# Performance work log

Measured on AMD Instinct MI355X. Metric: run time of the kernel, lower is better.

Reference implementation:

```python
import jax, jax.numpy as jnp
import numpy as np

B, D, H = 16384, 1024, 8
DH = D // H
LN_EPS = 1e-5


def setup_inputs() -> dict:
    key = jax.random.key(0)
    ks = jax.random.split(key, 16)
    s = 0.02  # weight init scale to keep softmax logits sane
    d = {}
    d['f40'] = jax.random.normal(ks[0], (B, D), jnp.float32)
    d['f100'] = jax.random.normal(ks[1], (B, D), jnp.float32)
    d['f200'] = jax.random.normal(ks[2], (B, D), jnp.float32)
    d['f400'] = jax.random.normal(ks[3], (B, D), jnp.float32)
    d['mag_emb'] = jax.random.normal(ks[4], (4, D), jnp.float32)
    i = 5
    for mag in ('100', '200', '400'):
        d[f'in_w_{mag}'] = jax.random.normal(ks[i], (3 * D, D), jnp.float32) * s
        d[f'in_b_{mag}'] = jnp.zeros((3 * D,), jnp.float32)
        d[f'out_w_{mag}'] = jax.random.normal(ks[i + 1], (D, D), jnp.float32) * s
        d[f'out_b_{mag}'] = jnp.zeros((D,), jnp.float32)
        d[f'ln_w_{mag}'] = jnp.ones((D,), jnp.float32)
        d[f'ln_b_{mag}'] = jnp.zeros((D,), jnp.float32)
        i += 2
    return d


def _layer_norm(x, w, b):
    m = jnp.mean(x, axis=-1, keepdims=True)
    v = jnp.mean(jnp.square(x - m), axis=-1, keepdims=True)
    return (x - m) * jax.lax.rsqrt(v + LN_EPS) * w + b


def _mha(q, kv, in_w, in_b, out_w, out_b):
    # q: [B,1,D], kv: [B,S,D]. Matches torch nn.MultiheadAttention (batch_first).
    S = kv.shape[1]
    wq, wk, wv = jnp.split(in_w, 3, axis=0)
    bq, bk, bv = jnp.split(in_b, 3)
    qp = (q @ wq.T + bq).reshape(B, 1, H, DH)
    kp = (kv @ wk.T + bk).reshape(B, S, H, DH)
    vp = (kv @ wv.T + bv).reshape(B, S, H, DH)
    scores = jnp.einsum('bqhd,bkhd->bhqk', qp, kp) / np.sqrt(DH).astype(np.float32)
    attn = jax.nn.softmax(scores, axis=-1)           # [B,H,1,S]
    out = jnp.einsum('bhqk,bkhd->bqhd', attn, vp).reshape(B, 1, D)
    out = (out @ out_w.T + out_b)[:, 0, :]           # [B,D]
    return out, attn.mean(axis=1)                     # weights averaged over heads: [B,1,S]


def reference(f40, f100, f200, f400, mag_emb,
              in_w_100, in_b_100, out_w_100, out_b_100, ln_w_100, ln_b_100,
              in_w_200, in_b_200, out_w_200, out_b_200, ln_w_200, ln_b_200,
              in_w_400, in_b_400, out_w_400, out_b_400, ln_w_400, ln_b_400):
    feats = (f40, f100, f200, f400)
    enh = [f + mag_emb[i] for i, f in enumerate(feats)]
    level_params = [
        (in_w_100, in_b_100, out_w_100, out_b_100, ln_w_100, ln_b_100),
        (in_w_200, in_b_200, out_w_200, out_b_200, ln_w_200, ln_b_200),
        (in_w_400, in_b_400, out_w_400, out_b_400, ln_w_400, ln_b_400),
    ]
    hier = [enh[0]]
    attn_maps = []
    for i, (iw, ib, ow, ob, lw, lb) in enumerate(level_params):
        ctx = jnp.stack(hier, axis=1)                 # [B, i+1, D]
        attended, w = _mha(enh[i + 1][:, None, :], ctx, iw, ib, ow, ob)
        fused = _layer_norm(enh[i + 1] + attended, lw, lb)
        hier.append(fused)
        attn_maps.append(w)
    return (hier[0], hier[1], hier[2], hier[3], attn_maps[0], attn_maps[1], attn_maps[2])
```

## Files before the change

### kernel.cpp

```cpp
#include <hip/hip_runtime.h>

typedef unsigned short u16;
typedef unsigned int u32;

#define NB 16384
#define ND 1024
static constexpr size_t BD = (size_t)NB * ND;
static constexpr size_t DD = (size_t)ND * ND;

typedef __attribute__((ext_vector_type(8))) short s16x8;
typedef __attribute__((ext_vector_type(4))) float f32x4;

__device__ __forceinline__ u16 f2bf(float f) {
  union { float f; u32 u; } v; v.f = f;
  return (u16)((v.u + 0x7fffu + ((v.u >> 16) & 1u)) >> 16);
}
__device__ __forceinline__ float asf(u32 u) {
  union { u32 u; float f; } v; v.u = u; return v.f;
}
__device__ __forceinline__ uint2 pack4(float a, float b, float c, float d) {
  uint2 p;
  p.x = (u32)f2bf(a) | ((u32)f2bf(b) << 16);
  p.y = (u32)f2bf(c) | ((u32)f2bf(d) << 16);
  return p;
}
__device__ __forceinline__ void load16bf(const u16* p, float* o) {
  const uint4* q = (const uint4*)p;
  uint4 u0 = q[0], u1 = q[1];
  u32 w[8] = {u0.x, u0.y, u0.z, u0.w, u1.x, u1.y, u1.z, u1.w};
#pragma unroll
  for (int i = 0; i < 8; ++i) {
    o[2 * i]     = asf(w[i] << 16);
    o[2 * i + 1] = asf(w[i] & 0xffff0000u);
  }
}
__device__ __forceinline__ void store16bf(u16* p, const float* o) {
  uint4 u0, u1;
  u0.x = (u32)f2bf(o[0])  | ((u32)f2bf(o[1])  << 16);
  u0.y = (u32)f2bf(o[2])  | ((u32)f2bf(o[3])  << 16);
  u0.z = (u32)f2bf(o[4])  | ((u32)f2bf(o[5])  << 16);
  u0.w = (u32)f2bf(o[6])  | ((u32)f2bf(o[7])  << 16);
  u1.x = (u32)f2bf(o[8])  | ((u32)f2bf(o[9])  << 16);
  u1.y = (u32)f2bf(o[10]) | ((u32)f2bf(o[11]) << 16);
  u1.z = (u32)f2bf(o[12]) | ((u32)f2bf(o[13]) << 16);
  u1.w = (u32)f2bf(o[14]) | ((u32)f2bf(o[15]) << 16);
  ((uint4*)p)[0] = u0;
  ((uint4*)p)[1] = u1;
}

#define G2L(gp, lp) __builtin_amdgcn_global_load_lds( \
    (__attribute__((address_space(1))) void*)(void*)(gp), \
    (__attribute__((address_space(3))) void*)(lp), 16, 0, 0)

template<int BF16_OUT>
__device__ __forceinline__ void gemm_core(
    const u16* __restrict__ A, const u16* __restrict__ Bm,
    const float* __restrict__ bias, void* __restrict__ Cp,
    int N, int K, int ldc, int row0, int col0)
{
  __shared__ __align__(16) u16 lA[128 * 64];
  __shared__ __align__(16) u16 lB[128 * 64];
  const int tid  = threadIdx.x;
  const int wave = tid >> 6;
  const int lane = tid & 63;
  const int wm = (wave >> 1) * 64;
  const int wn = (wave & 1) * 64;
  const int fr = lane & 15;
  const int fq = lane >> 4;
  const int srow = tid >> 3;
  const int scol = ((tid & 7) ^ (srow & 7)) * 8;

  f32x4 acc[4][4];
#pragma unroll
  for (int i = 0; i < 4; ++i)
#pragma unroll
    for (int j = 0; j < 4; ++j) acc[i][j] = (f32x4){0.f, 0.f, 0.f, 0.f};

  const u16* Abase = A  + (size_t)(row0 + srow) * K + scol;
  const u16* Bbase = Bm + (size_t)(col0 + srow) * K + scol;
  u16* lAw = lA + wave * 512;
  u16* lBw = lB + wave * 512;
  const int rsw = (fr & 7) << 3;

  for (int kt = 0; kt < K; kt += 64) {
#pragma unroll
    for (int c = 0; c < 4; ++c) {
      G2L(Abase + (size_t)(c * 32) * K + kt, lAw + c * 2048);
      G2L(Bbase + (size_t)(c * 32) * K + kt, lBw + c * 2048);
    }
    __syncthreads();

#pragma unroll
    for (int kk = 0; kk < 2; ++kk) {
      s16x8 af[4], bfr[4];
#pragma unroll
      for (int i = 0; i < 4; ++i) {
        af[i]  = *(const s16x8*)&lA[(wm + i * 16 + fr) * 64 + ((kk * 32 + fq * 8) ^ rsw)];
        bfr[i] = *(const s16x8*)&lB[(wn + i * 16 + fr) * 64 + ((kk * 32 + fq * 8) ^ rsw)];
      }
#pragma unroll
      for (int i = 0; i < 4; ++i)
#pragma unroll
        for (int j = 0; j < 4; ++j)
          acc[i][j] = __builtin_amdgcn_mfma_f32_16x16x32_bf16(af[i], bfr[j], acc[i][j], 0, 0, 0);
    }
    __syncthreads();
  }

#pragma unroll
  for (int i = 0; i < 4; ++i) {
#pragma unroll
    for (int j = 0; j < 4; ++j) {
      const int col = col0 + wn + j * 16 + fr;
      const float bb = bias ? bias[col] : 0.f;
#pragma unroll
      for (int r = 0; r < 4; ++r) {
        const int row = row0 + wm + i * 16 + fq * 4 + r;
        const float v = acc[i][j][r] + bb;
        if (BF16_OUT) ((u16*)Cp)[(size_t)row * ldc + col] = f2bf(v);
        else          ((float*)Cp)[(size_t)row * ldc + col] = v;
      }
    }
  }
}

__device__ __forceinline__ void swz_rowcol(int* row0, int* col0) {
  const int nwg = gridDim.x * gridDim.y;
  int wgid = blockIdx.y * gridDim.x + blockIdx.x;
  wgid = (wgid & 7) * (nwg >> 3) + (wgid >> 3);
  *row0 = (wgid / gridDim.x) * 128;
  *col0 = (wgid % gridDim.x) * 128;
}

template<int BF16_OUT>
__global__ __launch_bounds__(256, 3) void gemm_bt(
    const u16* __restrict__ A, const u16* __restrict__ Bm,
    const float* __restrict__ bias, void* __restrict__ Cp,
    int N, int K, int ldc)
{
  int row0, col0;
  swz_rowcol(&row0, &col0);
  gemm_core<BF16_OUT>(A, Bm, bias, Cp, N, K, ldc, row0, col0);
}

struct Ptr3 { const u16* a0; const u16* a1; const u16* a2;
              u16* c0; u16* c1; u16* c2; };

__global__ __launch_bounds__(256, 3) void kv_gemm(
    Ptr3 p, const u16* __restrict__ Bm, int K)
{
  int row0, col0;
  swz_rowcol(&row0, &col0);
  const u16* A; u16* C;
  if (blockIdx.z == 0)      { A = p.a0; C = p.c0; }
  else if (blockIdx.z == 1) { A = p.a1; C = p.c1; }
  else                      { A = p.a2; C = p.c2; }
  gemm_core<1>(A, Bm, nullptr, C, 2048, K, 2048, row0, col0);
}

__global__ __launch_bounds__(256) void prep_k(
    const float* __restrict__ f40, const float* __restrict__ f200,
    const float* __restrict__ f400, const float* __restrict__ mag,
    float* __restrict__ out0, u16* __restrict__ h0b,
    u16* __restrict__ e2b, u16* __restrict__ e3b)
{
  const size_t j = ((size_t)blockIdx.x * 256 + threadIdx.x) * 4;
  const int d = (int)(j & 1023);
  float4 m0 = *(const float4*)(mag + d);
  float4 m2 = *(const float4*)(mag + 2 * ND + d);
  float4 m3 = *(const float4*)(mag + 3 * ND + d);
  float4 a  = *(const float4*)(f40 + j);
  float4 c2 = *(const float4*)(f200 + j);
  float4 c3 = *(const float4*)(f400 + j);
  float4 h0;
  h0.x = a.x + m0.x; h0.y = a.y + m0.y; h0.z = a.z + m0.z; h0.w = a.w + m0.w;
  *(float4*)(out0 + j) = h0;
  *(uint2*)(h0b + j) = pack4(h0.x, h0.y, h0.z, h0.w);
  *(uint2*)(e2b + j) = pack4(c2.x + m2.x, c2.y + m2.y, c2.z + m2.z, c2.w + m2.w);
  *(uint2*)(e3b + j) = pack4(c3.x + m3.x, c3.y + m3.y, c3.z + m3.z, c3.w + m3.w);
}

__global__ __launch_bounds__(256) void ones_k(float* __restrict__ p) {
  p[blockIdx.x * 256 + threadIdx.x] = 1.0f;
}

__global__ __launch_bounds__(256) void convw_k(
    const float* __restrict__ iw, const float* __restrict__ ow,
    u16* __restrict__ wbf)
{
  const size_t j = ((size_t)blockIdx.x * 256 + threadIdx.x) * 4;
  const size_t IW = (size_t)3 * ND * ND;
  const float* src = (j < IW) ? (iw + j) : (ow + (j - IW));
  float4 v = *(const float4*)src;
  *(uint2*)(wbf + j) = pack4(v.x, v.y, v.z, v.w);
}

__global__ __launch_bounds__(256) void transpose_bf_k(
    const float* __restrict__ src, u16* __restrict__ dst)
{
  __shared__ float t[32][33];
  const int bx = blockIdx.x & 31, by = blockIdx.x >> 5;
  const int tx = threadIdx.x & 31, ty = threadIdx.x >> 5;
#pragma unroll
  for (int r = 0; r < 4; ++r)
    t[ty + r * 8][tx] = src[(size_t)(by * 32 + ty + r * 8) * ND + bx * 32 + tx];
  __syncthreads();
#pragma unroll
  for (int r = 0; r < 4; ++r)
    dst[(size_t)(bx * 32 + ty + r * 8) * ND + by * 32 + tx] = f2bf(t[tx][ty + r * 8]);
}

__global__ __launch_bounds__(256) void biasfold_k(
    const float* __restrict__ bv, const float* __restrict__ wo,
    const float* __restrict__ bo, float* __restrict__ c0)
{
  const int i = blockIdx.x;
  float s = 0.f;
  for (int k = threadIdx.x; k < ND; k += 256) s += bv[k] * wo[(size_t)i * ND + k];
#pragma unroll
  for (int m = 1; m <= 32; m <<= 1) s += __shfl_xor(s, m, 64);
  __shared__ float red[4];
  const int wv = threadIdx.x >> 6, ln = threadIdx.x & 63;
  if (ln == 0) red[wv] = s;
  __syncthreads();
  if (threadIdx.x == 0) c0[i] = bo[i] + red[0] + red[1] + red[2] + red[3];
}

template<int S>
__global__ __launch_bounds__(256) void attn_k(
    const u16* __restrict__ qp, const u16* __restrict__ kva,
    const u16* __restrict__ kvb, const u16* __restrict__ kvc,
    u16* __restrict__ att, float* __restrict__ amap)
{
  const int wave = threadIdx.x >> 6, lane = threadIdx.x & 63;
  const int b = blockIdx.x * 4 + wave;
  const int d0 = lane * 16;
  const u16* kv[3] = {kva, kvb, kvc};

  float q[16];
  load16bf(qp + (size_t)b * ND + d0, q);

  float sc[S];
  float mx = -1e30f;
#pragma unroll
  for (int s = 0; s < S; ++s) {
    float k[16];
    load16bf(kv[s] + (size_t)b * 2 * ND + d0, k);
    float dot = 0.f;
#pragma unroll
    for (int i = 0; i < 16; ++i) dot += q[i] * k[i];
    dot += __shfl_xor(dot, 1, 64);
    dot += __shfl_xor(dot, 2, 64);
    dot += __shfl_xor(dot, 4, 64);
    sc[s] = dot * 0.08838834764831845f;
    mx = fmaxf(mx, sc[s]);
  }
  float w_[S];
  float den = 0.f;
#pragma unroll
  for (int s = 0; s < S; ++s) { w_[s] = __expf(sc[s] - mx); den += w_[s]; }
  const float inv = 1.f / den;

  float o[16] = {0.f, 0.f, 0.f, 0.f, 0.f, 0.f, 0.f, 0.f,
                 0.f, 0.f, 0.f, 0.f, 0.f, 0.f, 0.f, 0.f};
#pragma unroll
  for (int s = 0; s < S; ++s) {
    float v[16];
    load16bf(kv[s] + (size_t)b * 2 * ND + ND + d0, v);
    const float ws = w_[s] * inv;
#pragma unroll
    for (int i = 0; i < 16; ++i) o[i] += ws * v[i];
  }
  store16bf(att + (size_t)b * ND + d0, o);

#pragma unroll
  for (int s = 0; s < S; ++s) {
    float t = w_[s] * inv;
    t += __shfl_xor(t, 8, 64);
    t += __shfl_xor(t, 16, 64);
    t += __shfl_xor(t, 32, 64);
    if (lane == 0) amap[(size_t)b * S + s] = t * 0.125f;
  }
}

__global__ __launch_bounds__(256) void ln_k(
    const float* __restrict__ f, const float* __restrict__ emb,
    const u16* __restrict__ ob, const float* __restrict__ lw,
    const float* __restrict__ lb, float* __restrict__ outp,
    u16* __restrict__ hbf)
{
  const int b = blockIdx.x, t = threadIdx.x;
  const int d = t * 4;
  const size_t off = (size_t)b * ND + d;
  float4 xf = *(const float4*)(f + off);
  float4 ef = *(const float4*)(emb + d);
  uint2 ov  = *(const uint2*)(ob + off);
  float o0 = asf(ov.x << 16), o1 = asf(ov.x & 0xffff0000u);
  float o2 = asf(ov.y << 16), o3 = asf(ov.y & 0xffff0000u);
  float x0 = xf.x + ef.x + o0;
  float x1 = xf.y + ef.y + o1;
  float x2 = xf.z + ef.z + o2;
  float x3 = xf.w + ef.w + o3;
  float s  = x0 + x1 + x2 + x3;
  float s2 = x0 * x0 + x1 * x1 + x2 * x2 + x3 * x3;
#pragma unroll
  for (int m = 1; m <= 32; m <<= 1) {
    s  += __shfl_xor(s,  m, 64);
    s2 += __shfl_xor(s2, m, 64);
  }
  __shared__ float red[8];
  const int wv = t >> 6, ln = t & 63;
  if (ln == 0) { red[wv] = s; red[4 + wv] = s2; }
  __syncthreads();
  s  = red[0] + red[1] + red[2] + red[3];
  s2 = red[4] + red[5] + red[6] + red[7];
  const float mean = s * (1.f / 1024.f);
  const float var  = s2 * (1.f / 1024.f) - mean * mean;
  const float r = rsqrtf(var + 1e-5f);
  float4 w4 = *(const float4*)(lw + d);
  float4 b4 = *(const float4*)(lb + d);
  float4 y;
  y.x = (x0 - mean) * r * w4.x + b4.x;
  y.y = (x1 - mean) * r * w4.y + b4.y;
  y.z = (x2 - mean) * r * w4.z + b4.z;
  y.w = (x3 - mean) * r * w4.w + b4.w;
  *(float4*)(outp + off) = y;
  if (hbf) *(uint2*)(hbf + off) = pack4(y.x, y.y, y.z, y.w);
}

extern "C" void kernel_launch(void* const* d_in, const int* in_sizes, int n_in,
                              void* d_out, int out_size, void* d_ws, size_t ws_size,
                              hipStream_t stream)
{
  const float* f40  = (const float*)d_in[0];
  const float* f100 = (const float*)d_in[1];
  const float* f200 = (const float*)d_in[2];
  const float* f400 = (const float*)d_in[3];
  const float* mag  = (const float*)d_in[4];
  const float* in_w[3]  = {(const float*)d_in[5],  (const float*)d_in[11], (const float*)d_in[17]};
  const float* in_b[3]  = {(const float*)d_in[6],  (const float*)d_in[12], (const float*)d_in[18]};
  const float* out_w[3] = {(const float*)d_in[7],  (const float*)d_in[13], (const float*)d_in[19]};
  const float* out_b[3] = {(const float*)d_in[8],  (const float*)d_in[14], (const float*)d_in[20]};
  const float* ln_w[3]  = {(const float*)d_in[9],  (const float*)d_in[15], (const float*)d_in[21]};
  const float* ln_b[3]  = {(const float*)d_in[10], (const float*)d_in[16], (const float*)d_in[22]};

  float* out = (float*)d_out;
  char* ws = (char*)d_ws;
  const size_t BF = BD * 2;
  u16* h0b  = (u16*)(ws);
  u16* h1b  = (u16*)(ws + BF);
  u16* h2b  = (u16*)(ws + 2 * BF);
  u16* qpb  = (u16*)(ws + 3 * BF);
  u16* attb = (u16*)(ws + 4 * BF);
  u16* kv0  = (u16*)(ws + 5 * BF);
  u16* kv1  = (u16*)(ws + 7 * BF);
  u16* kv2  = (u16*)(ws + 9 * BF);
  u16* wbf  = (u16*)(ws + 11 * BF);
  float* cs = (float*)(ws + 11 * BF + 8 * (1ull << 20));
  u16* e2b = kv1;
  u16* e3b = kv2;
  u16* hb[3] = {h0b, h1b, h2b};
  const float* f_lvl[3] = {f100, f200, f400};

  dim3 blk(256);
  prep_k<<<dim3((unsigned)(BD / 1024)), blk, 0, stream>>>(f40, f200, f400, mag, out, h0b, e2b, e3b);
  ones_k<<<dim3(NB / 256), blk, 0, stream>>>(out + 4 * BD);

  for (int l = 0; l < 3; ++l) {
    convw_k<<<dim3(4096), blk, 0, stream>>>(in_w[l], out_w[l], wbf);
    const u16* wq  = wbf;
    const u16* wkv = wbf + DD;
    const u16* wo  = wbf + 3 * DD;
    biasfold_k<<<dim3(1024), blk, 0, stream>>>(in_b[l] + 2 * ND, out_w[l], out_b[l], cs);

    if (l == 0) {
      u16* wvT = attb;
      u16* wvo = attb + DD;
      transpose_bf_k<<<dim3(1024), blk, 0, stream>>>(in_w[0] + 2 * DD, wvT);
      gemm_bt<1><<<dim3(8, 8), blk, 0, stream>>>(wo, wvT, nullptr, wvo, ND, ND, ND);
      gemm_bt<1><<<dim3(8, 128), blk, 0, stream>>>(h0b, wvo, cs, qpb, ND, ND, ND);
    } else {
      const u16* eb = (l == 1) ? e2b : e3b;
      gemm_bt<1><<<dim3(8, 128), blk, 0, stream>>>(eb, wq, in_b[l], qpb, ND, ND, ND);
      Ptr3 p = {hb[0], hb[1], hb[2], kv0, kv1, kv2};
      kv_gemm<<<dim3(16, 128, l + 1), blk, 0, stream>>>(p, wkv, ND);
      if (l == 1)
        attn_k<2><<<dim3(NB / 4), blk, 0, stream>>>(qpb, kv0, kv1, kv2, attb,
                                                    out + 4 * BD + NB);
      else
        attn_k<3><<<dim3(NB / 4), blk, 0, stream>>>(qpb, kv0, kv1, kv2, attb,
                                                    out + 4 * BD + 3 * NB);
      gemm_bt<1><<<dim3(8, 128), blk, 0, stream>>>(attb, wo, cs, qpb, ND, ND, ND);
    }
    ln_k<<<dim3(NB), blk, 0, stream>>>(f_lvl[l], mag + (size_t)(l + 1) * ND, qpb,
                                       ln_w[l], ln_b[l], out + (size_t)(l + 1) * BD,
                                       (l < 2) ? hb[l + 1] : nullptr);
  }
}
```

Before: 865.2 us.

## Switch GEMMs to 256x256 tiles with double-buffered LDS pipeline and 512 threads

Replaces the 128x128 single-buffered GEMM core with a 256x256 tile computed by 8 waves, each holding a 128x64 accumulator block. The LDS is double-buffered, with direct global-to-LDS loads issued two k-steps ahead, explicit vmcnt waits and raw barriers replacing __syncthreads. MFMA issue priority is raised during the compute phase. This aims to raise arithmetic intensity and overlap loads with MFMA. In exchange it uses 128KB of LDS and many more accumulator registers per block, which lowers occupancy, and the small 1024x1024 weight GEMM now runs on only 16 blocks.

New measurement: 960.4 us. 11.0% more time.

```diff
diff --git a/kernel.cpp b/kernel.cpp
--- a/kernel.cpp
+++ b/kernel.cpp
@@ -52,71 +52,97 @@
     (__attribute__((address_space(1))) void*)(void*)(gp), \
     (__attribute__((address_space(3))) void*)(lp), 16, 0, 0)
 
+__device__ __forceinline__ void stage256(
+    const u16* __restrict__ Abase, const u16* __restrict__ Bbase,
+    u16* ldsA, u16* ldsB, int wave, int K, int kt)
+{
+#pragma unroll
+  for (int c = 0; c < 4; ++c) {
+    G2L(Abase + (size_t)(c * 64) * K + kt, ldsA + c * 4096 + wave * 512);
+    G2L(Bbase + (size_t)(c * 64) * K + kt, ldsB + c * 4096 + wave * 512);
+  }
+}
+
 template<int BF16_OUT>
-__device__ __forceinline__ void gemm_core(
+__device__ __forceinline__ void gemm256_core(
     const u16* __restrict__ A, const u16* __restrict__ Bm,
     const float* __restrict__ bias, void* __restrict__ Cp,
     int N, int K, int ldc, int row0, int col0)
 {
-  __shared__ __align__(16) u16 lA[128 * 64];
-  __shared__ __align__(16) u16 lB[128 * 64];
+  __shared__ __align__(16) u16 lA[2][256 * 64];
+  __shared__ __align__(16) u16 lB[2][256 * 64];
   const int tid  = threadIdx.x;
   const int wave = tid >> 6;
   const int lane = tid & 63;
-  const int wm = (wave >> 1) * 64;
-  const int wn = (wave & 1) * 64;
+  const int wm = wave >> 2;
+  const int wn = wave & 3;
   const int fr = lane & 15;
   const int fq = lane >> 4;
-  const int srow = tid >> 3;
-  const int scol = ((tid & 7) ^ (srow & 7)) * 8;
-
-  f32x4 acc[4][4];
-#pragma unroll
-  for (int i = 0; i < 4; ++i)
+  const int swr = (fr & 7) * 8;
+
+  const int g_r  = wave * 8 + (lane >> 3);
+  const int scol = ((lane & 7) ^ (lane >> 3)) * 8;
+  const u16* Abase = A  + (size_t)(row0 + g_r) * K + scol;
+  const u16* Bbase = Bm + (size_t)(col0 + g_r) * K + scol;
+
+  f32x4 acc[8][4];
+#pragma unroll
+  for (int i = 0; i < 8; ++i)
 #pragma unroll
     for (int j = 0; j < 4; ++j) acc[i][j] = (f32x4){0.f, 0.f, 0.f, 0.f};
 
-  const u16* Abase = A  + (size_t)(row0 + srow) * K + scol;
-  const u16* Bbase = Bm + (size_t)(col0 + srow) * K + scol;
-  u16* lAw = lA + wave * 512;
-  u16* lBw = lB + wave * 512;
-  const int rsw = (fr & 7) << 3;
-
-  for (int kt = 0; kt < K; kt += 64) {
-#pragma unroll
-    for (int c = 0; c < 4; ++c) {
-      G2L(Abase + (size_t)(c * 32) * K + kt, lAw + c * 2048);
-      G2L(Bbase + (size_t)(c * 32) * K + kt, lBw + c * 2048);
+  const int NT = K >> 6;
+  stage256(Abase, Bbase, &lA[0][0], &lB[0][0], wave, K, 0);
+  stage256(Abase, Bbase, &lA[1][0], &lB[1][0], wave, K, 64);
+
+  for (int t = 0; t < NT; ++t) {
+    if (t < NT - 1) { asm volatile("s_waitcnt vmcnt(8)" ::: "memory"); }
+    else            { asm volatile("s_waitcnt vmcnt(0)" ::: "memory"); }
+    __builtin_amdgcn_sched_barrier(0);
+    __builtin_amdgcn_s_barrier();
+    __builtin_amdgcn_sched_barrier(0);
+
+    const u16* bA = &lA[t & 1][0];
+    const u16* bB = &lB[t & 1][0];
+
+    s16x8 bf_[4][2];
+#pragma unroll
+    for (int ni = 0; ni < 4; ++ni) {
+      const int rb = wn * 64 + ni * 16 + fr;
+      bf_[ni][0] = *(const s16x8*)&bB[rb * 64 + ((fq * 8) ^ swr)];
+      bf_[ni][1] = *(const s16x8*)&bB[rb * 64 + ((32 + fq * 8) ^ swr)];
     }
-    __syncthreads();
-
-#pragma unroll
-    for (int kk = 0; kk < 2; ++kk) {
-      s16x8 af[4], bfr[4];
-#pragma unroll
-      for (int i = 0; i < 4; ++i) {
-        af[i]  = *(const s16x8*)&lA[(wm + i * 16 + fr) * 64 + ((kk * 32 + fq * 8) ^ rsw)];
-        bfr[i] = *(const s16x8*)&lB[(wn + i * 16 + fr) * 64 + ((kk * 32 + fq * 8) ^ rsw)];
+    __builtin_amdgcn_s_setprio(1);
+#pragma unroll
+    for (int mi = 0; mi < 8; ++mi) {
+      const int ra = wm * 128 + mi * 16 + fr;
+      s16x8 a0 = *(const s16x8*)&bA[ra * 64 + ((fq * 8) ^ swr)];
+      s16x8 a1 = *(const s16x8*)&bA[ra * 64 + ((32 + fq * 8) ^ swr)];
+#pragma unroll
+      for (int ni = 0; ni < 4; ++ni) {
+        acc[mi][ni] = __builtin_amdgcn_mfma_f32_16x16x32_bf16(a0, bf_[ni][0], acc[mi][ni], 0, 0, 0);
+        acc[mi][ni] = __builtin_amdgcn_mfma_f32_16x16x32_bf16(a1, bf_[ni][1], acc[mi][ni], 0, 0, 0);
       }
-#pragma unroll
-      for (int i = 0; i < 4; ++i)
-#pragma unroll
-        for (int j = 0; j < 4; ++j)
-          acc[i][j] = __builtin_amdgcn_mfma_f32_16x16x32_bf16(af[i], bfr[j], acc[i][j], 0, 0, 0);
     }
-    __syncthreads();
-  }
-
-#pragma unroll
-  for (int i = 0; i < 4; ++i) {
-#pragma unroll
-    for (int j = 0; j < 4; ++j) {
-      const int col = col0 + wn + j * 16 + fr;
+    __builtin_amdgcn_s_setprio(0);
+
+    __builtin_amdgcn_sched_barrier(0);
+    __builtin_amdgcn_s_barrier();
+    __builtin_amdgcn_sched_barrier(0);
+    if (t + 2 < NT)
+      stage256(Abase, Bbase, &lA[t & 1][0], &lB[t & 1][0], wave, K, (t + 2) * 64);
+  }
+
+#pragma unroll
+  for (int mi = 0; mi < 8; ++mi) {
+#pragma unroll
+    for (int ni = 0; ni < 4; ++ni) {
+      const int col = col0 + wn * 64 + ni * 16 + fr;
       const float bb = bias ? bias[col] : 0.f;
 #pragma unroll
       for (int r = 0; r < 4; ++r) {
-        const int row = row0 + wm + i * 16 + fq * 4 + r;
-        const float v = acc[i][j][r] + bb;
+        const int row = row0 + wm * 128 + mi * 16 + fq * 4 + r;
+        const float v = acc[mi][ni][r] + bb;
         if (BF16_OUT) ((u16*)Cp)[(size_t)row * ldc + col] = f2bf(v);
         else          ((float*)Cp)[(size_t)row * ldc + col] = v;
       }
@@ -128,25 +154,25 @@
   const int nwg = gridDim.x * gridDim.y;
   int wgid = blockIdx.y * gridDim.x + blockIdx.x;
   wgid = (wgid & 7) * (nwg >> 3) + (wgid >> 3);
-  *row0 = (wgid / gridDim.x) * 128;
-  *col0 = (wgid % gridDim.x) * 128;
+  *row0 = (wgid / gridDim.x) * 256;
+  *col0 = (wgid % gridDim.x) * 256;
 }
 
 template<int BF16_OUT>
-__global__ __launch_bounds__(256, 3) void gemm_bt(
+__global__ __launch_bounds__(512, 2) void gemm256_bt(
     const u16* __restrict__ A, const u16* __restrict__ Bm,
     const float* __restrict__ bias, void* __restrict__ Cp,
     int N, int K, int ldc)
 {
   int row0, col0;
   swz_rowcol(&row0, &col0);
-  gemm_core<BF16_OUT>(A, Bm, bias, Cp, N, K, ldc, row0, col0);
+  gemm256_core<BF16_OUT>(A, Bm, bias, Cp, N, K, ldc, row0, col0);
 }
 
 struct Ptr3 { const u16* a0; const u16* a1; const u16* a2;
               u16* c0; u16* c1; u16* c2; };
 
-__global__ __launch_bounds__(256, 3) void kv_gemm(
+__global__ __launch_bounds__(512, 2) void kv256_gemm(
     Ptr3 p, const u16* __restrict__ Bm, int K)
 {
   int row0, col0;
@@ -155,7 +181,7 @@
   if (blockIdx.z == 0)      { A = p.a0; C = p.c0; }
   else if (blockIdx.z == 1) { A = p.a1; C = p.c1; }
   else                      { A = p.a2; C = p.c2; }
-  gemm_core<1>(A, Bm, nullptr, C, 2048, K, 2048, row0, col0);
+  gemm256_core<1>(A, Bm, nullptr, C, 2048, K, 2048, row0, col0);
 }
 
 __global__ __launch_bounds__(256) void prep_k(
@@ -362,7 +388,7 @@
   u16* hb[3] = {h0b, h1b, h2b};
   const float* f_lvl[3] = {f100, f200, f400};
 
-  dim3 blk(256);
+  dim3 blk(256), blk5(512);
   prep_k<<<dim3((unsigned)(BD / 1024)), blk, 0, stream>>>(f40, f200, f400, mag, out, h0b, e2b, e3b);
   ones_k<<<dim3(NB / 256), blk, 0, stream>>>(out + 4 * BD);
 
@@ -377,20 +403,20 @@
       u16* wvT = attb;
       u16* wvo = attb + DD;
       transpose_bf_k<<<dim3(1024), blk, 0, stream>>>(in_w[0] + 2 * DD, wvT);
-      gemm_bt<1><<<dim3(8, 8), blk, 0, stream>>>(wo, wvT, nullptr, wvo, ND, ND, ND);
-      gemm_bt<1><<<dim3(8, 128), blk, 0, stream>>>(h0b, wvo, cs, qpb, ND, ND, ND);
+      gemm256_bt<1><<<dim3(4, 4), blk5, 0, stream>>>(wo, wvT, nullptr, wvo, ND, ND, ND);
+      gemm256_bt<1><<<dim3(4, 64), blk5, 0, stream>>>(h0b, wvo, cs, qpb, ND, ND, ND);
     } else {
       const u16* eb = (l == 1) ? e2b : e3b;
-      gemm_bt<1><<<dim3(8, 128), blk, 0, stream>>>(eb, wq, in_b[l], qpb, ND, ND, ND);
+      gemm256_bt<1><<<dim3(4, 64), blk5, 0, stream>>>(eb, wq, in_b[l], qpb, ND, ND, ND);
       Ptr3 p = {hb[0], hb[1], hb[2], kv0, kv1, kv2};
-      kv_gemm<<<dim3(16, 128, l + 1), blk, 0, stream>>>(p, wkv, ND);
+      kv256_gemm<<<dim3(8, 64, l + 1), blk5, 0, stream>>>(p, wkv, ND);
       if (l == 1)
         attn_k<2><<<dim3(NB / 4), blk, 0, stream>>>(qpb, kv0, kv1, kv2, attb,
                                                     out + 4 * BD + NB);
       else
         attn_k<3><<<dim3(NB / 4), blk, 0, stream>>>(qpb, kv0, kv1, kv2, attb,
                                                     out + 4 * BD + 3 * NB);
-      gemm_bt<1><<<dim3(8, 128), blk, 0, stream>>>(attb, wo, cs, qpb, ND, ND, ND);
+      gemm256_bt<1><<<dim3(4, 64), blk5, 0, stream>>>(attb, wo, cs, qpb, ND, ND, ND);
     }
     ln_k<<<dim3(NB), blk, 0, stream>>>(f_lvl[l], mag + (size_t)(l + 1) * ND, qpb,
                                        ln_w[l], ln_b[l], out + (size_t)(l + 1) * BD,
```

## Replace KV projection GEMM with 256x256-tile 8-wave pipelined kernel

Applied to the files above, without the earlier changes.

Swaps the 128x128-tile, 256-thread KV projection GEMM for a 256x256-tile, 512-thread kernel. The new kernel double-buffers LDS with direct global-to-LDS loads and splits each k-step into four MFMA phases, interleaving fragment reads, barriers and prefetch of the next tile under raised wave priority. The larger tile gives more reuse per byte loaded, cutting global and LDS traffic for this large GEMM. In exchange it uses 64KB of LDS per block and more accumulator registers, which may lower occupancy. A dead, incomplete stub kernel (kv8p_gemm) is also left in the file.

After: 868.1 us. No clear change (+0.3%).

```diff
diff --git a/kernel.cpp b/kernel.cpp
--- a/kernel.cpp
+++ b/kernel.cpp
@@ -124,12 +124,12 @@
   }
 }
 
-__device__ __forceinline__ void swz_rowcol(int* row0, int* col0) {
+__device__ __forceinline__ void swz_rowcol(int* row0, int* col0, int tile) {
   const int nwg = gridDim.x * gridDim.y;
   int wgid = blockIdx.y * gridDim.x + blockIdx.x;
   wgid = (wgid & 7) * (nwg >> 3) + (wgid >> 3);
-  *row0 = (wgid / gridDim.x) * 128;
-  *col0 = (wgid % gridDim.x) * 128;
+  *row0 = (wgid / gridDim.x) * tile;
+  *col0 = (wgid % gridDim.x) * tile;
 }
 
 template<int BF16_OUT>
@@ -139,23 +139,201 @@
     int N, int K, int ldc)
 {
   int row0, col0;
-  swz_rowcol(&row0, &col0);
+  swz_rowcol(&row0, &col0, 128);
   gemm_core<BF16_OUT>(A, Bm, bias, Cp, N, K, ldc, row0, col0);
 }
 
-struct Ptr3 { const u16* a0; const u16* a1; const u16* a2;
-              u16* c0; u16* c1; u16* c2; };
-
-__global__ __launch_bounds__(256, 3) void kv_gemm(
-    Ptr3 p, const u16* __restrict__ Bm, int K)
+__global__ __launch_bounds__(512, 2) void kv8p_gemm(
+    const u16* __restrict__ a0, const u16* __restrict__ a1,
+    const u16* __restrict__ a2, u16* __restrict__ c0,
+    u16* __restrict__ c1, u16* __restrict__ c2, int K)
 {
   int row0, col0;
-  swz_rowcol(&row0, &col0);
+  swz_rowcol(&row0, &col0, 256);
   const u16* A; u16* C;
-  if (blockIdx.z == 0)      { A = p.a0; C = p.c0; }
-  else if (blockIdx.z == 1) { A = p.a1; C = p.c1; }
-  else                      { A = p.a2; C = p.c2; }
-  gemm_core<1>(A, Bm, nullptr, C, 2048, K, 2048, row0, col0);
+  if (blockIdx.z == 0)      { A = a0; C = c0; }
+  else if (blockIdx.z == 1) { A = a1; C = c1; }
+  else                      { A = a2; C = c2; }
+  const int ldc = 2048;
+
+  __shared__ __align__(16) u16 lA[2][256 * 64];
+  __shared__ __align__(16) u16 lB[2][256 * 64];
+  const int tid  = threadIdx.x;
+  const int wave = tid >> 6;
+  const int lane = tid & 63;
+  const int wm = wave >> 2;
+  const int wn = wave & 3;
+  const int fr = lane & 15;
+  const int fq = lane >> 4;
+  const int swr = (fr & 7) * 8;
+
+  const int srow = wave * 8 + (lane >> 3);
+  const int scol = ((lane & 7) ^ (lane >> 3)) * 8;
+  const u16* Asrc = A                          + (size_t)(row0 + srow) * K + scol;
+  const u16* Bsrc =  nullptr;
+  (void)Bsrc;
+  C[0] = C[0];
+}
+
+__global__ __launch_bounds__(512, 2) void kv8p_gemm2(
+    const u16* __restrict__ a0, const u16* __restrict__ a1,
+    const u16* __restrict__ a2, const u16* __restrict__ Bm,
+    u16* __restrict__ c0, u16* __restrict__ c1, u16* __restrict__ c2, int K)
+{
+  int row0, col0;
+  swz_rowcol(&row0, &col0, 256);
+  const u16* A; u16* C;
+  if (blockIdx.z == 0)      { A = a0; C = c0; }
+  else if (blockIdx.z == 1) { A = a1; C = c1; }
+  else                      { A = a2; C = c2; }
+  const int ldc = 2048;
+
+  __shared__ __align__(16) u16 lA[2][256 * 64];
+  __shared__ __align__(16) u16 lB[2][256 * 64];
+  const int tid  = threadIdx.x;
+  const int wave = tid >> 6;
+  const int lane = tid & 63;
+  const int wm = wave >> 2;
+  const int wn = wave & 3;
+  const int fr = lane & 15;
+  const int fq = lane >> 4;
+  const int swr = (fr & 7) * 8;
+
+  const int srow = wave * 8 + (lane >> 3);
+  const int scol = ((lane & 7) ^ (lane >> 3)) * 8;
+  const u16* Asrc = A  + (size_t)(row0 + srow) * K + scol;
+  const u16* Bsrc = Bm + (size_t)(col0 + srow) * K + scol;
+
+#define STG_A(b, h, kt) { \
+    G2L(Asrc + (size_t)((h) * 128)      * K + (kt), &lA[b][(h) * 8192        + wave * 512]); \
+    G2L(Asrc + (size_t)((h) * 128 + 64) * K + (kt), &lA[b][(h) * 8192 + 4096 + wave * 512]); }
+#define STG_B(b, h, kt) { \
+    G2L(Bsrc + (size_t)((h) * 128)      * K + (kt), &lB[b][(h) * 8192        + wave * 512]); \
+    G2L(Bsrc + (size_t)((h) * 128 + 64) * K + (kt), &lB[b][(h) * 8192 + 4096 + wave * 512]); }
+
+  f32x4 acc[8][4];
+#pragma unroll
+  for (int i = 0; i < 8; ++i)
+#pragma unroll
+    for (int j = 0; j < 4; ++j) acc[i][j] = (f32x4){0.f, 0.f, 0.f, 0.f};
+
+  const int NT = K >> 6;
+
+  STG_A(0, 0, 0);  STG_A(0, 1, 0);  STG_B(0, 0, 0);  STG_B(0, 1, 0);
+  STG_A(1, 0, 64); STG_A(1, 1, 64); STG_B(1, 0, 64); STG_B(1, 1, 64);
+  asm volatile("s_waitcnt vmcnt(8)" ::: "memory");
+  __builtin_amdgcn_s_barrier();
+
+  for (int t = 0; t < NT; ++t) {
+    const int bt = t & 1;
+    const u16* bA = &lA[bt][0];
+    const u16* bB = &lB[bt][0];
+    const int k2 = (t + 2) * 64;
+    const bool more = (t + 2) < NT;
+    s16x8 aF[4][2], bF0[2][2], bF1[2][2];
+
+#pragma unroll
+    for (int i = 0; i < 4; ++i) {
+      const int ra = wm * 128 + i * 16 + fr;
+      aF[i][0] = *(const s16x8*)&bA[ra * 64 + ((fq * 8) ^ swr)];
+      aF[i][1] = *(const s16x8*)&bA[ra * 64 + ((32 + fq * 8) ^ swr)];
+    }
+#pragma unroll
+    for (int j = 0; j < 2; ++j) {
+      const int rb = wn * 64 + j * 16 + fr;
+      bF0[j][0] = *(const s16x8*)&bB[rb * 64 + ((fq * 8) ^ swr)];
+      bF0[j][1] = *(const s16x8*)&bB[rb * 64 + ((32 + fq * 8) ^ swr)];
+    }
+    __builtin_amdgcn_sched_barrier(0);
+    __builtin_amdgcn_s_barrier();
+    asm volatile("s_waitcnt lgkmcnt(0)" ::: "memory");
+    __builtin_amdgcn_sched_barrier(0);
+    __builtin_amdgcn_s_setprio(1);
+#pragma unroll
+    for (int i = 0; i < 4; ++i)
+#pragma unroll
+      for (int j = 0; j < 2; ++j) {
+        acc[i][j] = __builtin_amdgcn_mfma_f32_16x16x32_bf16(aF[i][0], bF0[j][0], acc[i][j], 0, 0, 0);
+        acc[i][j] = __builtin_amdgcn_mfma_f32_16x16x32_bf16(aF[i][1], bF0[j][1], acc[i][j], 0, 0, 0);
+      }
+    __builtin_amdgcn_s_setprio(0);
+    __builtin_amdgcn_sched_barrier(0);
+
+#pragma unroll
+    for (int j = 0; j < 2; ++j) {
+      const int rb = wn * 64 + 32 + j * 16 + fr;
+      bF1[j][0] = *(const s16x8*)&bB[rb * 64 + ((fq * 8) ^ swr)];
+      bF1[j][1] = *(const s16x8*)&bB[rb * 64 + ((32 + fq * 8) ^ swr)];
+    }
+    __builtin_amdgcn_sched_barrier(0);
+    __builtin_amdgcn_s_barrier();
+    asm volatile("s_waitcnt lgkmcnt(0)" ::: "memory");
+    __builtin_amdgcn_sched_barrier(0);
+    __builtin_amdgcn_s_setprio(1);
+#pragma unroll
+    for (int i = 0; i < 4; ++i)
+#pragma unroll
+      for (int j = 0; j < 2; ++j) {
+        acc[i][2 + j] = __builtin_amdgcn_mfma_f32_16x16x32_bf16(aF[i][0], bF1[j][0], acc[i][2 + j], 0, 0, 0);
+        acc[i][2 + j] = __builtin_amdgcn_mfma_f32_16x16x32_bf16(aF[i][1], bF1[j][1], acc[i][2 + j], 0, 0, 0);
+      }
+    __builtin_amdgcn_s_setprio(0);
+    __builtin_amdgcn_sched_barrier(0);
+
+    if (more) { STG_B(bt, 0, k2); STG_B(bt, 1, k2); }
+#pragma unroll
+    for (int i = 0; i < 4; ++i) {
+      const int ra = wm * 128 + 64 + i * 16 + fr;
+      aF[i][0] = *(const s16x8*)&bA[ra * 64 + ((fq * 8) ^ swr)];
+      aF[i][1] = *(const s16x8*)&bA[ra * 64 + ((32 + fq * 8) ^ swr)];
+    }
+    __builtin_amdgcn_sched_barrier(0);
+    __builtin_amdgcn_s_barrier();
+    asm volatile("s_waitcnt lgkmcnt(0)" ::: "memory");
+    __builtin_amdgcn_sched_barrier(0);
+    __builtin_amdgcn_s_setprio(1);
+#pragma unroll
+    for (int i = 0; i < 4; ++i)
+#pragma unroll
+      for (int j = 0; j < 2; ++j) {
+        acc[4 + i][j] = __builtin_amdgcn_mfma_f32_16x16x32_bf16(aF[i][0], bF0[j][0], acc[4 + i][j], 0, 0, 0);
+        acc[4 + i][j] = __builtin_amdgcn_mfma_f32_16x16x32_bf16(aF[i][1], bF0[j][1], acc[4 + i][j], 0, 0, 0);
+      }
+    __builtin_amdgcn_s_setprio(0);
+    __builtin_amdgcn_sched_barrier(0);
+
+    if (more) { STG_A(bt, 0, k2); STG_A(bt, 1, k2); }
+    __builtin_amdgcn_sched_barrier(0);
+    if (more) { asm volatile("s_waitcnt vmcnt(8)" ::: "memory"); }
+    else      { asm volatile("s_waitcnt vmcnt(0)" ::: "memory"); }
+    __builtin_amdgcn_s_barrier();
+    __builtin_amdgcn_sched_barrier(0);
+    __builtin_amdgcn_s_setprio(1);
+#pragma unroll
+    for (int i = 0; i < 4; ++i)
+#pragma unroll
+      for (int j = 0; j < 2; ++j) {
+        acc[4 + i][2 + j] = __builtin_amdgcn_mfma_f32_16x16x32_bf16(aF[i][0], bF1[j][0], acc[4 + i][2 + j], 0, 0, 0);
+        acc[4 + i][2 + j] = __builtin_amdgcn_mfma_f32_16x16x32_bf16(aF[i][1], bF1[j][1], acc[4 + i][2 + j], 0, 0, 0);
+      }
+    __builtin_amdgcn_s_setprio(0);
+    __builtin_amdgcn_sched_barrier(0);
+  }
+#undef STG_A
+#undef STG_B
+
+#pragma unroll
+  for (int mi = 0; mi < 8; ++mi) {
+#pragma unroll
+    for (int ni = 0; ni < 4; ++ni) {
+      const int col = col0 + wn * 64 + ni * 16 + fr;
+#pragma unroll
+      for (int r = 0; r < 4; ++r) {
+        const int row = row0 + wm * 128 + mi * 16 + fq * 4 + r;
+        C[(size_t)row * ldc + col] = f2bf(acc[mi][ni][r]);
+      }
+    }
+  }
 }
 
 __global__ __launch_bounds__(256) void prep_k(
@@ -362,7 +540,7 @@
   u16* hb[3] = {h0b, h1b, h2b};
   const float* f_lvl[3] = {f100, f200, f400};
 
-  dim3 blk(256);
+  dim3 blk(256), blk5(512);
   prep_k<<<dim3((unsigned)(BD / 1024)), blk, 0, stream>>>(f40, f200, f400, mag, out, h0b, e2b, e3b);
   ones_k<<<dim3(NB / 256), blk, 0, stream>>>(out + 4 * BD);
 
@@ -382,8 +560,8 @@
     } else {
       const u16* eb = (l == 1) ? e2b : e3b;
       gemm_bt<1><<<dim3(8, 128), blk, 0, stream>>>(eb, wq, in_b[l], qpb, ND, ND, ND);
-      Ptr3 p = {hb[0], hb[1], hb[2], kv0, kv1, kv2};
-      kv_gemm<<<dim3(16, 128, l + 1), blk, 0, stream>>>(p, wkv, ND);
+      kv8p_gemm2<<<dim3(8, 64, l + 1), blk5, 0, stream>>>(hb[0], hb[1], hb[2], wkv,
+                                                          kv0, kv1, kv2, ND);
       if (l == 1)
         attn_k<2><<<dim3(NB / 4), blk, 0, stream>>>(qpb, kv0, kv1, kv2, attb,
                                                     out + 4 * BD + NB);
```

## Add 256x256-tile 8-wave KV GEMM with phased LDS pipeline for level 3

Applied to the files above, without the earlier changes.

Adds a new KV projection GEMM kernel that uses 512 threads and 256x256 output tiles, with double-buffered swizzled LDS, interleaved global-to-LDS loads split across four compute phases, explicit waitcnt/barriers, and setprio around MFMA clusters. It is used only for the third level's KV projection (three context slices); level 2 keeps the old 128x128 kernel. Larger tiles raise arithmetic intensity and cut redundant global loads, but use 64KB of LDS per block, giving fewer blocks per CU (gridDim 8x64x3) and relying on hand-tuned scheduling.

After: 870.1 us. About the same (+0.6%).

```diff
diff --git a/kernel.cpp b/kernel.cpp
--- a/kernel.cpp
+++ b/kernel.cpp
@@ -124,12 +124,12 @@
   }
 }
 
-__device__ __forceinline__ void swz_rowcol(int* row0, int* col0) {
+__device__ __forceinline__ void swz_rowcol(int* row0, int* col0, int tile) {
   const int nwg = gridDim.x * gridDim.y;
   int wgid = blockIdx.y * gridDim.x + blockIdx.x;
   wgid = (wgid & 7) * (nwg >> 3) + (wgid >> 3);
-  *row0 = (wgid / gridDim.x) * 128;
-  *col0 = (wgid % gridDim.x) * 128;
+  *row0 = (wgid / gridDim.x) * tile;
+  *col0 = (wgid % gridDim.x) * tile;
 }
 
 template<int BF16_OUT>
@@ -139,7 +139,7 @@
     int N, int K, int ldc)
 {
   int row0, col0;
-  swz_rowcol(&row0, &col0);
+  swz_rowcol(&row0, &col0, 128);
   gemm_core<BF16_OUT>(A, Bm, bias, Cp, N, K, ldc, row0, col0);
 }
 
@@ -150,12 +150,149 @@
     Ptr3 p, const u16* __restrict__ Bm, int K)
 {
   int row0, col0;
-  swz_rowcol(&row0, &col0);
+  swz_rowcol(&row0, &col0, 128);
   const u16* A; u16* C;
   if (blockIdx.z == 0)      { A = p.a0; C = p.c0; }
   else if (blockIdx.z == 1) { A = p.a1; C = p.c1; }
   else                      { A = p.a2; C = p.c2; }
   gemm_core<1>(A, Bm, nullptr, C, 2048, K, 2048, row0, col0);
+}
+
+__global__ __launch_bounds__(512, 2) void kv8_gemm(
+    const u16* __restrict__ a0, const u16* __restrict__ a1,
+    const u16* __restrict__ a2, const u16* __restrict__ Bm,
+    u16* __restrict__ c0, u16* __restrict__ c1, u16* __restrict__ c2, int K)
+{
+  int row0, col0;
+  swz_rowcol(&row0, &col0, 256);
+  const u16* A; u16* C;
+  if (blockIdx.z == 0)      { A = a0; C = c0; }
+  else if (blockIdx.z == 1) { A = a1; C = c1; }
+  else                      { A = a2; C = c2; }
+  const int ldc = 2048;
+
+  __shared__ __align__(16) u16 lA[2][256 * 64];
+  __shared__ __align__(16) u16 lB[2][256 * 64];
+  const int tid  = threadIdx.x;
+  const int wave = tid >> 6;
+  const int lane = tid & 63;
+  const int wm = wave >> 2;
+  const int wn = wave & 3;
+  const int fr = lane & 15;
+  const int fq = lane >> 4;
+  const int swr = (fr & 7) * 8;
+
+  const int srow = wave * 8 + (lane >> 3);
+  const int scol = ((lane & 7) ^ (lane >> 3)) * 8;
+  const u16* Asrc = A  + (size_t)(row0 + srow) * K + scol;
+  const u16* Bsrc = Bm + (size_t)(col0 + srow) * K + scol;
+
+#define SA(BUF, CC, KT) G2L(Asrc + (size_t)((CC) * 64) * K + (KT), &lA[BUF][(CC) * 4096 + wave * 512])
+#define SB(BUF, CC, KT) G2L(Bsrc + (size_t)((CC) * 64) * K + (KT), &lB[BUF][(CC) * 4096 + wave * 512])
+#define RD_A(MH, BUF) { \
+    const u16* bA_ = &lA[BUF][0]; \
+    for (int i = 0; i < 4; ++i) { \
+      const int ra = wm * 128 + (MH) * 64 + i * 16 + fr; \
+      aF[i][0] = *(const s16x8*)&bA_[ra * 64 + ((fq * 8) ^ swr)]; \
+      aF[i][1] = *(const s16x8*)&bA_[ra * 64 + ((32 + fq * 8) ^ swr)]; \
+    } }
+#define RD_B(DST, NH, BUF) { \
+    const u16* bB_ = &lB[BUF][0]; \
+    for (int j = 0; j < 2; ++j) { \
+      const int rb = wn * 64 + (NH) * 32 + j * 16 + fr; \
+      DST[j][0] = *(const s16x8*)&bB_[rb * 64 + ((fq * 8) ^ swr)]; \
+      DST[j][1] = *(const s16x8*)&bB_[rb * 64 + ((32 + fq * 8) ^ swr)]; \
+    } }
+#define CLUSTER(MH, NH, BFR) \
+    for (int i = 0; i < 4; ++i) \
+      for (int j = 0; j < 2; ++j) { \
+        acc[(MH) * 4 + i][(NH) * 2 + j] = __builtin_amdgcn_mfma_f32_16x16x32_bf16( \
+            aF[i][0], BFR[j][0], acc[(MH) * 4 + i][(NH) * 2 + j], 0, 0, 0); \
+        acc[(MH) * 4 + i][(NH) * 2 + j] = __builtin_amdgcn_mfma_f32_16x16x32_bf16( \
+            aF[i][1], BFR[j][1], acc[(MH) * 4 + i][(NH) * 2 + j], 0, 0, 0); \
+      }
+#define PH_TAIL(MH, NH, BFR) \
+    __builtin_amdgcn_sched_barrier(0); \
+    __builtin_amdgcn_s_barrier(); \
+    asm volatile("s_waitcnt lgkmcnt(0)" ::: "memory"); \
+    __builtin_amdgcn_sched_barrier(0); \
+    __builtin_amdgcn_s_setprio(1); \
+    CLUSTER(MH, NH, BFR); \
+    __builtin_amdgcn_s_setprio(0); \
+    __builtin_amdgcn_sched_barrier(0); \
+    __builtin_amdgcn_s_barrier(); \
+    __builtin_amdgcn_sched_barrier(0);
+
+  f32x4 acc[8][4];
+#pragma unroll
+  for (int i = 0; i < 8; ++i)
+#pragma unroll
+    for (int j = 0; j < 4; ++j) acc[i][j] = (f32x4){0.f, 0.f, 0.f, 0.f};
+
+  const int NT = K >> 6;
+
+  SA(0, 0, 0); SA(0, 1, 0); SA(0, 2, 0); SA(0, 3, 0);
+  SB(0, 0, 0); SB(0, 1, 0); SB(0, 2, 0); SB(0, 3, 0);
+  SA(1, 0, 64); SA(1, 2, 64);
+  SB(1, 0, 64); SB(1, 1, 64); SB(1, 2, 64); SB(1, 3, 64);
+  asm volatile("s_waitcnt vmcnt(6)" ::: "memory");
+  __builtin_amdgcn_s_barrier();
+
+#pragma unroll 1
+  for (int t = 0; t < NT; t += 2) {
+    const int kt1 = (t + 1) * 64, kt2 = (t + 2) * 64, kt3 = (t + 3) * 64;
+    const bool m2 = (t + 2) < NT, m3 = (t + 3) < NT;
+    s16x8 aF[4][2], bF0[2][2], bF1[2][2];
+
+    RD_A(0, 0); RD_B(bF0, 0, 0);
+    SA(1, 1, kt1); SA(1, 3, kt1);
+    PH_TAIL(0, 0, bF0);
+    RD_B(bF1, 1, 0);
+    if (m2) { SA(0, 0, kt2); SA(0, 2, kt2); }
+    PH_TAIL(0, 1, bF1);
+    RD_A(1, 0);
+    if (m2) { SB(0, 0, kt2); SB(0, 1, kt2); }
+    PH_TAIL(1, 0, bF0);
+    if (m2) { SB(0, 2, kt2); SB(0, 3, kt2); }
+    __builtin_amdgcn_sched_barrier(0);
+    if (m2) { asm volatile("s_waitcnt vmcnt(6)" ::: "memory"); }
+    else    { asm volatile("s_waitcnt vmcnt(0)" ::: "memory"); }
+    PH_TAIL(1, 1, bF1);
+
+    RD_A(0, 1); RD_B(bF0, 0, 1);
+    if (m2) { SA(0, 1, kt2); SA(0, 3, kt2); }
+    PH_TAIL(0, 0, bF0);
+    RD_B(bF1, 1, 1);
+    if (m3) { SA(1, 0, kt3); SA(1, 2, kt3); }
+    PH_TAIL(0, 1, bF1);
+    RD_A(1, 1);
+    if (m3) { SB(1, 0, kt3); SB(1, 1, kt3); }
+    PH_TAIL(1, 0, bF0);
+    if (m3) { SB(1, 2, kt3); SB(1, 3, kt3); }
+    __builtin_amdgcn_sched_barrier(0);
+    if (m3) { asm volatile("s_waitcnt vmcnt(6)" ::: "memory"); }
+    else    { asm volatile("s_waitcnt vmcnt(0)" ::: "memory"); }
+    PH_TAIL(1, 1, bF1);
+  }
+#undef SA
+#undef SB
+#undef RD_A
+#undef RD_B
+#undef CLUSTER
+#undef PH_TAIL
+
+#pragma unroll
+  for (int mi = 0; mi < 8; ++mi) {
+#pragma unroll
+    for (int ni = 0; ni < 4; ++ni) {
+      const int col = col0 + wn * 64 + ni * 16 + fr;
+#pragma unroll
+      for (int r = 0; r < 4; ++r) {
+        const int row = row0 + wm * 128 + mi * 16 + fq * 4 + r;
+        C[(size_t)row * ldc + col] = f2bf(acc[mi][ni][r]);
+      }
+    }
+  }
 }
 
 __global__ __launch_bounds__(256) void prep_k(
@@ -362,7 +499,7 @@
   u16* hb[3] = {h0b, h1b, h2b};
   const float* f_lvl[3] = {f100, f200, f400};
 
-  dim3 blk(256);
+  dim3 blk(256), blk5(512);
   prep_k<<<dim3((unsigned)(BD / 1024)), blk, 0, stream>>>(f40, f200, f400, mag, out, h0b, e2b, e3b);
   ones_k<<<dim3(NB / 256), blk, 0, stream>>>(out + 4 * BD);
 
@@ -382,8 +519,13 @@
     } else {
       const u16* eb = (l == 1) ? e2b : e3b;
       gemm_bt<1><<<dim3(8, 128), blk, 0, stream>>>(eb, wq, in_b[l], qpb, ND, ND, ND);
-      Ptr3 p = {hb[0], hb[1], hb[2], kv0, kv1, kv2};
-      kv_gemm<<<dim3(16, 128, l + 1), blk, 0, stream>>>(p, wkv, ND);
+      if (l == 1) {
+        Ptr3 p = {hb[0], hb[1], hb[2], kv0, kv1, kv2};
+        kv_gemm<<<dim3(16, 128, 2), blk, 0, stream>>>(p, wkv, ND);
+      } else {
+        kv8_gemm<<<dim3(8, 64, 3), blk5, 0, stream>>>(hb[0], hb[1], hb[2], wkv,
+                                                      kv0, kv1, kv2, ND);
+      }
       if (l == 1)
         attn_k<2><<<dim3(NB / 4), blk, 0, stream>>>(qpb, kv0, kv1, kv2, attb,
                                                     out + 4 * BD + NB);
```
